# Performance work log

Measured on AMD Instinct MI355X. Metric: run time of the kernel, lower is better.

Reference implementation:

```python
import jax, jax.numpy as jnp
import numpy as np
import math

NODE_DIM = 256
HIDDEN = 128
HEADS = 8
HEAD_DIM = HIDDEN // HEADS
SCALE = math.sqrt(HEAD_DIM)
EPS_DIST = 1e-6
EPS_NORM = 1e-6
LN_EPS = 1e-5


def setup_inputs() -> dict:
    key = jax.random.key(0)
    ks = jax.random.split(key, 16)
    B, N = 2, 768
    node_feats = jax.random.normal(ks[0], (B, N, NODE_DIM), dtype=jnp.float32)
    positions = jax.random.normal(ks[1], (B, N, 2), dtype=jnp.float32)
    mask = jax.random.randint(ks[2], (B, N), 0, 2).astype(bool)
    s = 0.05
    return {
        "node_feats": node_feats,
        "positions": positions,
        "mask": mask,
        "Wq": jax.random.normal(ks[3], (NODE_DIM, HIDDEN), dtype=jnp.float32) * s,
        "Wk": jax.random.normal(ks[4], (NODE_DIM, HIDDEN), dtype=jnp.float32) * s,
        "Wv": jax.random.normal(ks[5], (NODE_DIM, HIDDEN), dtype=jnp.float32) * s,
        "W1": jax.random.normal(ks[6], (3, HIDDEN), dtype=jnp.float32) * s,
        "b1": jnp.zeros((HIDDEN,), dtype=jnp.float32),
        "W2": jax.random.normal(ks[7], (HIDDEN, HIDDEN), dtype=jnp.float32) * s,
        "b2": jnp.zeros((HIDDEN,), dtype=jnp.float32),
        "Wo": jax.random.normal(ks[8], (HIDDEN, NODE_DIM), dtype=jnp.float32) * s,
        "bo": jnp.zeros((NODE_DIM,), dtype=jnp.float32),
        "gamma": jnp.ones((NODE_DIM,), dtype=jnp.float32),
        "beta": jnp.zeros((NODE_DIM,), dtype=jnp.float32),
    }


def reference(node_feats, positions, mask, Wq, Wk, Wv, W1, b1, W2, b2, Wo, bo, gamma, beta):
    B, N, _ = node_feats.shape
    # projections -> [B, H, N, hd]
    q = (node_feats @ Wq).reshape(B, N, HEADS, HEAD_DIM).transpose(0, 2, 1, 3)
    k = (node_feats @ Wk).reshape(B, N, HEADS, HEAD_DIM).transpose(0, 2, 1, 3)
    v = (node_feats @ Wv).reshape(B, N, HEADS, HEAD_DIM).transpose(0, 2, 1, 3)

    # pairwise geometry: deltas [B, N, N, 2]
    deltas = positions[:, :, None, :] - positions[:, None, :, :]
    sq = (deltas ** 2).sum(-1)
    distances = jnp.sqrt(sq + EPS_DIST)  # [B, N, N]
    # F.normalize: divide by norm clamped to eps
    norm = jnp.sqrt(sq)[..., None]
    direction = deltas / jnp.maximum(norm, EPS_NORM)
    edge_geom = jnp.concatenate([direction, distances[..., None]], axis=-1)  # [B,N,N,3]

    # edge MLP -> [B, N, N, HIDDEN] (exact GELU as torch default)
    h = jax.nn.gelu(edge_geom @ W1 + b1, approximate=False)
    edge_bias = (h @ W2 + b2).reshape(B, N, N, HEADS, HEAD_DIM)
    # mean over head_dim, permute to [B, H, N, N]
    bias = edge_bias.mean(-1).transpose(0, 3, 1, 2)

    scores = jnp.einsum('bhid,bhjd->bhij', q, k) / SCALE + bias

    key_mask = mask[:, None, None, :]  # [B,1,1,N]
    neg = jnp.finfo(scores.dtype).min
    scores = jnp.where(key_mask, scores, neg)
    valid_key_rows = jnp.any(key_mask, axis=-1, keepdims=True)  # [B,1,1,1]

    mx = scores.max(axis=-1, keepdims=True)
    mx = jnp.where(valid_key_rows, mx, 0.0)
    scores = jnp.where(valid_key_rows, scores - mx, 0.0)
    w = jax.nn.softmax(scores, axis=-1)
    w = jnp.where(valid_key_rows, w, 0.0)
    w = jnp.nan_to_num(w, nan=0.0, posinf=0.0, neginf=0.0)
    # query mask
    w = w * mask[:, None, :, None].astype(w.dtype)
    # dropout is identity at eval time

    agg = jnp.einsum('bhij,bhjd->bhid', w, v)  # [B,H,N,hd]
    agg = agg.transpose(0, 2, 1, 3).reshape(B, N, HIDDEN)
    agg = agg @ Wo + bo

    mf = mask[..., None].astype(node_feats.dtype)
    agg = agg * mf
    nf = node_feats * mf

    x = nf + agg
    mu = x.mean(-1, keepdims=True)
    var = ((x - mu) ** 2).mean(-1, keepdims=True)
    return (x - mu) / jnp.sqrt(var + LN_EPS) * gamma + beta
```

## Files before the change

kernel.cpp:

```cpp
#include <hip/hip_runtime.h>
#include <float.h>
#include <math.h>

#define NODE_DIM 256
#define HIDDEN   128
#define HEADS    8
#define HEAD_DIM 16
#define NB       768
#define BATCH    2
#define NNODES   (BATCH * NB)
#define SEP      776

typedef _Float16 f16;
typedef _Float16 h2 __attribute__((ext_vector_type(2)));
union F2H { float f; h2 h; unsigned u; };
union V4H { float4 f; h2 h[4]; };

__device__ __forceinline__ float gelu_f(float u) {
  float u2 = u * u;
  float e  = __builtin_amdgcn_exp2f(u * fmaf(u2, -0.10294357f, -2.3022090f));
  return u * __builtin_amdgcn_rcpf(1.0f + e);
}

__global__ __launch_bounds__(256) void prep_kernel(
    const float* __restrict__ nf, const float* __restrict__ pos,
    const int* __restrict__ mask,
    const float* __restrict__ Wq, const float* __restrict__ Wk,
    const float* __restrict__ Wv, const float* __restrict__ W1,
    const float* __restrict__ b1, const float* __restrict__ W2,
    const float* __restrict__ b2, const float* __restrict__ Wo,
    float* __restrict__ qc, f16* __restrict__ kTcH, f16* __restrict__ vcH,
    unsigned* __restrict__ WoP,
    float* __restrict__ P, float* __restrict__ b2m,
    float* __restrict__ pcx, float* __restrict__ pcy,
    int* __restrict__ vlist, int* __restrict__ mlist, int* __restrict__ cnt) {
  int blk = blockIdx.x, t = threadIdx.x;

  if (blk < NNODES / 4) {
    int n0 = blk * 4;
    int b = n0 / NB;
    int lo = n0 - b * NB;
    __shared__ int accv;
    if (t == 0) accv = 0;
    __syncthreads();
    for (int jb = 0; jb < lo; jb += 256) {
      int j = jb + t;
      int mv = (j < lo) && (mask[b * NB + j] != 0);
      unsigned long long ball = __ballot(mv);
      if ((t & 63) == 0) atomicAdd(&accv, __popcll(ball));
    }
    __syncthreads();
    int cb = accv;
    int m0 = mask[n0] != 0, m1 = mask[n0 + 1] != 0, m2 = mask[n0 + 2] != 0,
        m3 = mask[n0 + 3] != 0;
    int civ[4] = {cb, cb + m0, cb + m0 + m1, cb + m0 + m1 + m2};
    int mv4[4] = {m0, m1, m2, m3};

    const float* x0 = nf + (size_t)(n0 + 0) * NODE_DIM;
    const float* x1 = nf + (size_t)(n0 + 1) * NODE_DIM;
    const float* x2 = nf + (size_t)(n0 + 2) * NODE_DIM;
    const float* x3 = nf + (size_t)(n0 + 3) * NODE_DIM;
    for (int id = t; id < 3 * HIDDEN; id += 256) {
      int m = id >> 7, c = id & 127;
      const float* W = (m == 0) ? Wq : (m == 1) ? Wk : Wv;
      float a0 = 0.f, a1 = 0.f, a2 = 0.f, a3 = 0.f;
      float e0 = 0.f, e1 = 0.f, e2 = 0.f, e3 = 0.f;
#pragma unroll 8
      for (int kk = 0; kk < NODE_DIM; kk += 2) {
        float w0 = W[kk * HIDDEN + c];
        float w1 = W[(kk + 1) * HIDDEN + c];
        a0 = fmaf(x0[kk], w0, a0);  e0 = fmaf(x0[kk + 1], w1, e0);
        a1 = fmaf(x1[kk], w0, a1);  e1 = fmaf(x1[kk + 1], w1, e1);
        a2 = fmaf(x2[kk], w0, a2);  e2 = fmaf(x2[kk + 1], w1, e2);
        a3 = fmaf(x3[kk], w0, a3);  e3 = fmaf(x3[kk + 1], w1, e3);
      }
      float acc[4] = {a0 + e0, a1 + e1, a2 + e2, a3 + e3};
#pragma unroll
      for (int n = 0; n < 4; ++n) {
        if (mv4[n]) {
          int slot = b * NB + civ[n];
          if (m == 0)      qc[(size_t)slot * HIDDEN + c] = acc[n];
          else if (m == 1) kTcH[((size_t)b * HIDDEN + c) * NB + civ[n]] = (f16)acc[n];
          else             vcH[(size_t)slot * HIDDEN + c] = (f16)acc[n];
        }
      }
    }
  } else if (blk < NNODES / 4 + 2) {
    int b = blk - NNODES / 4;
    __shared__ int wcnt[4];
    __shared__ int base2[2];
    if (t < 2) base2[t] = 0;
    __syncthreads();
    int lane = t & 63, w = t >> 6;
    for (int iter = 0; iter < NB / 256; ++iter) {
      int j = iter * 256 + t;
      int mv = mask[b * NB + j] != 0;
      unsigned long long ball = __ballot(mv);
      if (lane == 0) wcnt[w] = __popcll(ball);
      __syncthreads();
      int pv = 0;
      for (int i = 0; i < w; ++i) pv += wcnt[i];
      int pin = (lane == 0) ? 0 : __popcll(ball & (~0ull >> (64 - lane)));
      if (mv) {
        int p = base2[0] + pv + pin;
        vlist[b * NB + p] = j;
        pcx[b * NB + p] = pos[(b * NB + j) * 2];
        pcy[b * NB + p] = pos[(b * NB + j) * 2 + 1];
      } else {
        int pm = base2[1] + (w * 64 - pv) + (lane - pin);
        mlist[b * NB + pm] = j;
      }
      __syncthreads();
      if (t == 0) {
        int tot = wcnt[0] + wcnt[1] + wcnt[2] + wcnt[3];
        base2[0] += tot;
        base2[1] += 256 - tot;
      }
      __syncthreads();
    }
    int nv = base2[0];
    if (t == 0) cnt[b] = nv;
    int nvp8 = (nv + 7) & ~7;
    if (t < HIDDEN)
      for (int col = nv; col < nvp8; ++col)
        kTcH[((size_t)b * HIDDEN + t) * NB + col] = (f16)0.0f;
  } else if (blk == NNODES / 4 + 2) {
    __shared__ float w2s[HIDDEN * HEADS];
    for (int idx = t; idx < HIDDEN * HEADS; idx += 256) {
      int c = idx >> 3, h = idx & 7;
      float s = 0.0f;
      for (int d = 0; d < HEAD_DIM; ++d) s += W2[c * HIDDEN + h * HEAD_DIM + d];
      w2s[idx] = s * (1.0f / 16.0f);
    }
    if (t < HEADS) {
      float s = 0.0f;
      for (int d = 0; d < HEAD_DIM; ++d) s += b2[t * HEAD_DIM + d];
      b2m[t] = s * (1.0f / 16.0f);
    }
    __syncthreads();
    if (t < HIDDEN) {
      float* Pr = P + t * 8;
      Pr[0] = W1[t];
      Pr[1] = W1[HIDDEN + t];
      Pr[2] = W1[2 * HIDDEN + t];
      Pr[3] = b1[t];
      f16* ph = (f16*)(Pr + 4);
#pragma unroll
      for (int h = 0; h < HEADS; ++h) ph[h] = (f16)w2s[t * 8 + h];
    }
  } else {
    for (int k2 = 0; k2 < 64; ++k2) {
      F2H w;
      w.h = (h2){(f16)Wo[(2 * k2) * NODE_DIM + t],
                 (f16)Wo[(2 * k2 + 1) * NODE_DIM + t]};
      WoP[k2 * 256 + t] = w.u;
    }
  }
}

__global__ __launch_bounds__(256) void attn_kernel(
    const float* __restrict__ pcx, const float* __restrict__ pcy,
    const int* __restrict__ cnt, const int* __restrict__ vlist,
    const int* __restrict__ mlist, const float* __restrict__ P,
    const float* __restrict__ b2m, const float* __restrict__ qc,
    const f16* __restrict__ kTcH, const f16* __restrict__ vcH,
    const unsigned* __restrict__ WoP,
    const float* __restrict__ nf, const float* __restrict__ bo,
    const float* __restrict__ gamma, const float* __restrict__ beta,
    float* __restrict__ out) {
  int b = blockIdx.x & 1, ci = blockIdx.x >> 1;
  int t = threadIdx.x;
  int nv = cnt[b];
  if (ci >= nv) {
    int node = b * NB + mlist[b * NB + (ci - nv)];
    out[(size_t)node * NODE_DIM + t] = beta[t];
    return;
  }
  int node = b * NB + vlist[b * NB + ci];
  int slot = b * NB + ci;

  __shared__ __align__(16) unsigned char smem[21760];
  f16*   sE    = (f16*)smem;
  float* qs    = (float*)(smem + 12416);
  float* partD = (float*)(smem + 12928);
  float* aggL  = (float*)(smem + 21120);
  float* red   = (float*)(smem + 21632);
  float* invs  = (float*)(smem + 21664);

  if (t < HIDDEN) qs[t] = qc[(size_t)slot * HIDDEN + t];
  float pix = pcx[slot], piy = pcy[slot];
  __syncthreads();

  {
    int h = t >> 5, l = t & 31;
    const f16* kb = kTcH + ((size_t)b * HIDDEN + h * 16) * NB;
    h2 qp[16];
#pragma unroll
    for (int r = 0; r < 16; ++r) {
      f16 qh = (f16)qs[h * 16 + r];
      qp[r] = (h2){qh, qh};
    }
    h2 sc4 = {(f16)0.25f, (f16)0.25f};
    f16 bhh = (f16)b2m[h];
    h2 bh2 = {bhh, bhh};
    int n8 = (nv + 7) >> 3;
    for (int j8 = l; j8 < n8; j8 += 32) {
      h2 acc[4] = {{0, 0}, {0, 0}, {0, 0}, {0, 0}};
#pragma unroll
      for (int r = 0; r < 16; ++r) {
        V4H kv;
        kv.f = *(const float4*)(kb + (size_t)r * NB + j8 * 8);
        acc[0] += qp[r] * kv.h[0];
        acc[1] += qp[r] * kv.h[1];
        acc[2] += qp[r] * kv.h[2];
        acc[3] += qp[r] * kv.h[3];
      }
      V4H res;
#pragma unroll
      for (int p = 0; p < 4; ++p) res.h[p] = acc[p] * sc4 + bh2;
      *(float4*)(sE + h * SEP + j8 * 8) = res.f;
    }
  }
  __syncthreads();

#pragma unroll
  for (int sl = 0; sl < 3; ++sl) {
    int k0 = t + sl * 256;
    if (k0 < nv) {
      int s0 = b * NB + k0;
      float dx = pix - pcx[s0], dy = piy - pcy[s0];
      float sq = fmaf(dx, dx, dy * dy);
      float dist = __builtin_amdgcn_sqrtf(sq + 1e-6f);
      float inv  = fminf(__builtin_amdgcn_rsqf(sq), 1e6f);
      float ux = dx * inv, uy = dy * inv;
      h2 bacc[4] = {{0, 0}, {0, 0}, {0, 0}, {0, 0}};
#pragma unroll 4
      for (int c = 0; c < HIDDEN; ++c) {
        const float4* Pc = (const float4*)(P + c * 8);
        float4 p0 = Pc[0], pw = Pc[1];
        float g = gelu_f(fmaf(ux, p0.x, fmaf(uy, p0.y, fmaf(dist, p0.z, p0.w))));
        f16 gh = (f16)g;
        h2 gg = {gh, gh};
        F2H w0, w1, w2, w3;
        w0.f = pw.x; w1.f = pw.y; w2.f = pw.z; w3.f = pw.w;
        bacc[0] += gg * w0.h;
        bacc[1] += gg * w1.h;
        bacc[2] += gg * w2.h;
        bacc[3] += gg * w3.h;
      }
      f16* row = sE + k0;
#pragma unroll
      for (int p = 0; p < 4; ++p) {
        row[(2 * p + 0) * SEP] = (f16)(row[(2 * p + 0) * SEP] + bacc[p].x);
        row[(2 * p + 1) * SEP] = (f16)(row[(2 * p + 1) * SEP] + bacc[p].y);
      }
    }
  }
  __syncthreads();

  {
    int h = t >> 5, l = t & 31;
    f16* row = sE + h * SEP;
    float m = -FLT_MAX;
    for (int jj = l; jj < nv; jj += 32) m = fmaxf(m, (float)row[jj]);
    for (int off = 16; off; off >>= 1) m = fmaxf(m, __shfl_down(m, off, 32));
    m = __shfl(m, 0, 32);
    float s = 0.0f;
    for (int jj = l; jj < nv; jj += 32) {
      float e = __expf((float)row[jj] - m);
      row[jj] = (f16)e;
      s += e;
    }
    for (int off = 16; off; off >>= 1) s += __shfl_down(s, off, 32);
    if (l == 0) invs[h] = 1.0f / s;
  }
  __syncthreads();

  {
    int o8 = t & 15, g = t >> 4;
    int h = o8 >> 1;
    h2 acc[4] = {{0, 0}, {0, 0}, {0, 0}, {0, 0}};
    for (int jj = g; jj < nv; jj += 16) {
      V4H vv;
      vv.f = *(const float4*)(vcH + (size_t)(b * NB + jj) * HIDDEN + o8 * 8);
      f16 w = sE[h * SEP + jj];
      h2 ww = {w, w};
      acc[0] += ww * vv.h[0];
      acc[1] += ww * vv.h[1];
      acc[2] += ww * vv.h[2];
      acc[3] += ww * vv.h[3];
    }
    float* pd = partD + g * HIDDEN + o8 * 8;
    pd[0] = (float)acc[0].x; pd[1] = (float)acc[0].y;
    pd[2] = (float)acc[1].x; pd[3] = (float)acc[1].y;
    pd[4] = (float)acc[2].x; pd[5] = (float)acc[2].y;
    pd[6] = (float)acc[3].x; pd[7] = (float)acc[3].y;
  }
  __syncthreads();
  if (t < HIDDEN) {
    float s = 0.0f;
#pragma unroll
    for (int g = 0; g < 16; ++g) s += partD[g * HIDDEN + t];
    aggL[t] = s * invs[t >> 4];
  }
  __syncthreads();

  {
    float y0 = bo[t], y1 = 0.f;
    const unsigned* wp = WoP + t;
    const float2* a2 = (const float2*)aggL;
#pragma unroll 4
    for (int k2 = 0; k2 < 64; ++k2) {
      F2H w;
      w.u = wp[(size_t)k2 * 256];
      float2 a = a2[k2];
      y0 = fmaf(a.x, (float)w.h.x, y0);
      y1 = fmaf(a.y, (float)w.h.y, y1);
    }
    float y = y0 + y1;
    float xv = nf[(size_t)node * NODE_DIM + t] + y;
    float s = xv, s2 = xv * xv;
    for (int off = 32; off; off >>= 1) {
      s += __shfl_down(s, off, 64);
      s2 += __shfl_down(s2, off, 64);
    }
    if ((t & 63) == 0) { red[t >> 6] = s; red[4 + (t >> 6)] = s2; }
    __syncthreads();
    s  = red[0] + red[1] + red[2] + red[3];
    s2 = red[4] + red[5] + red[6] + red[7];
    float mu = s * (1.0f / NODE_DIM);
    float var = fmaxf(s2 * (1.0f / NODE_DIM) - mu * mu, 0.0f);
    out[(size_t)node * NODE_DIM + t] =
        (xv - mu) * rsqrtf(var + 1e-5f) * gamma[t] + beta[t];
  }
}

extern "C" void kernel_launch(void* const* d_in, const int* in_sizes, int n_in,
                              void* d_out, int out_size, void* d_ws, size_t ws_size,
                              hipStream_t stream) {
  const float* nf    = (const float*)d_in[0];
  const float* pos   = (const float*)d_in[1];
  const int*   mask  = (const int*)  d_in[2];
  const float* Wq    = (const float*)d_in[3];
  const float* Wk    = (const float*)d_in[4];
  const float* Wv    = (const float*)d_in[5];
  const float* W1    = (const float*)d_in[6];
  const float* b1    = (const float*)d_in[7];
  const float* W2    = (const float*)d_in[8];
  const float* b2    = (const float*)d_in[9];
  const float* Wo    = (const float*)d_in[10];
  const float* bo    = (const float*)d_in[11];
  const float* gamma = (const float*)d_in[12];
  const float* beta  = (const float*)d_in[13];

  const int QKV = NNODES * HIDDEN;

  float*    ws   = (float*)d_ws;
  float*    qc   = ws;
  f16*      kTcH = (f16*)(qc + QKV);
  f16*      vcH  = kTcH + QKV;
  unsigned* WoP  = (unsigned*)(vcH + QKV);
  float*    P    = (float*)(WoP + 64 * 256);
  float*    b2m  = P + HIDDEN * 8;
  float*    pcx  = b2m + 8;
  float*    pcy  = pcx + NNODES;
  int*      vlist= (int*)(pcy + NNODES);
  int*      mlist= vlist + NNODES;
  int*      cnt  = mlist + NNODES;

  prep_kernel<<<NNODES / 4 + 4, 256, 0, stream>>>(
      nf, pos, mask, Wq, Wk, Wv, W1, b1, W2, b2, Wo,
      qc, kTcH, vcH, WoP, P, b2m, pcx, pcy, vlist, mlist, cnt);
  attn_kernel<<<NNODES, 256, 0, stream>>>(
      pcx, pcy, cnt, vlist, mlist, P, b2m, qc, kTcH, vcH, WoP,
      nf, bo, gamma, beta, (float*)d_out);
}
```

Measured before the change: 136.3 us.

## Process two query nodes per attention block to reuse K, V and Wo loads

Each attention block now handles two consecutive query slots instead of one, halving the grid. K tiles, V rows, edge-MLP weights and Wo are loaded once and applied to both queries, which cuts global and L2 traffic per query. The cost is double the shared memory and registers per block, which can reduce occupancy, and fewer blocks (768) to spread across the CUs. The softmax is regrouped to 16 lanes per head-query pair, and masked-out partner slots are written with beta.

```diff
diff --git a/kernel.cpp b/kernel.cpp
--- a/kernel.cpp
+++ b/kernel.cpp
@@ -10,6 +10,7 @@
 #define BATCH    2
 #define NNODES   (BATCH * NB)
 #define SEP      776
+#define SEQ      (HEADS * SEP)
 
 typedef _Float16 f16;
 typedef _Float16 h2 __attribute__((ext_vector_type(2)));
@@ -168,57 +169,77 @@
     const float* __restrict__ nf, const float* __restrict__ bo,
     const float* __restrict__ gamma, const float* __restrict__ beta,
     float* __restrict__ out) {
-  int b = blockIdx.x & 1, ci = blockIdx.x >> 1;
+  int blk = blockIdx.x;
+  int b = blk & 1, ci0 = (blk >> 1) * 2, ci1 = ci0 + 1;
   int t = threadIdx.x;
   int nv = cnt[b];
-  if (ci >= nv) {
-    int node = b * NB + mlist[b * NB + (ci - nv)];
-    out[(size_t)node * NODE_DIM + t] = beta[t];
+
+  if (ci0 >= nv) {
+    float bt = beta[t];
+    int nodeA = b * NB + mlist[b * NB + (ci0 - nv)];
+    int nodeB = b * NB + mlist[b * NB + (ci1 - nv)];
+    out[(size_t)nodeA * NODE_DIM + t] = bt;
+    out[(size_t)nodeB * NODE_DIM + t] = bt;
     return;
   }
-  int node = b * NB + vlist[b * NB + ci];
-  int slot = b * NB + ci;
-
-  __shared__ __align__(16) unsigned char smem[21760];
+  bool v1 = ci1 < nv;
+  int slot0 = b * NB + ci0;
+  int slot1 = b * NB + (v1 ? ci1 : ci0);
+  int node0 = b * NB + vlist[slot0 - b * NB + b * NB];
+  node0 = b * NB + vlist[b * NB + ci0];
+  int node1 = v1 ? (b * NB + vlist[b * NB + ci1]) : -1;
+
+  __shared__ __align__(16) unsigned char smem[43392];
   f16*   sE    = (f16*)smem;
-  float* qs    = (float*)(smem + 12416);
-  float* partD = (float*)(smem + 12928);
-  float* aggL  = (float*)(smem + 21120);
-  float* red   = (float*)(smem + 21632);
-  float* invs  = (float*)(smem + 21664);
-
-  if (t < HIDDEN) qs[t] = qc[(size_t)slot * HIDDEN + t];
-  float pix = pcx[slot], piy = pcy[slot];
+  float* qs    = (float*)(smem + 24832);
+  float* partD = (float*)(smem + 25856);
+  float* aggL  = (float*)(smem + 42240);
+  float* red   = (float*)(smem + 43264);
+  float* invs  = (float*)(smem + 43328);
+
+  if (t < HIDDEN) {
+    qs[t]          = qc[(size_t)slot0 * HIDDEN + t];
+    qs[HIDDEN + t] = qc[(size_t)slot1 * HIDDEN + t];
+  }
+  float pix0 = pcx[slot0], piy0 = pcy[slot0];
+  float pix1 = pcx[slot1], piy1 = pcy[slot1];
   __syncthreads();
 
   {
     int h = t >> 5, l = t & 31;
     const f16* kb = kTcH + ((size_t)b * HIDDEN + h * 16) * NB;
-    h2 qp[16];
+    h2 qp0[16], qp1[16];
 #pragma unroll
     for (int r = 0; r < 16; ++r) {
-      f16 qh = (f16)qs[h * 16 + r];
-      qp[r] = (h2){qh, qh};
+      f16 q0 = (f16)qs[h * 16 + r], q1 = (f16)qs[HIDDEN + h * 16 + r];
+      qp0[r] = (h2){q0, q0};
+      qp1[r] = (h2){q1, q1};
     }
     h2 sc4 = {(f16)0.25f, (f16)0.25f};
     f16 bhh = (f16)b2m[h];
     h2 bh2 = {bhh, bhh};
     int n8 = (nv + 7) >> 3;
     for (int j8 = l; j8 < n8; j8 += 32) {
-      h2 acc[4] = {{0, 0}, {0, 0}, {0, 0}, {0, 0}};
+      h2 a0[4] = {{0,0},{0,0},{0,0},{0,0}};
+      h2 a1[4] = {{0,0},{0,0},{0,0},{0,0}};
 #pragma unroll
       for (int r = 0; r < 16; ++r) {
         V4H kv;
         kv.f = *(const float4*)(kb + (size_t)r * NB + j8 * 8);
-        acc[0] += qp[r] * kv.h[0];
-        acc[1] += qp[r] * kv.h[1];
-        acc[2] += qp[r] * kv.h[2];
-        acc[3] += qp[r] * kv.h[3];
-      }
-      V4H res;
-#pragma unroll
-      for (int p = 0; p < 4; ++p) res.h[p] = acc[p] * sc4 + bh2;
-      *(float4*)(sE + h * SEP + j8 * 8) = res.f;
+#pragma unroll
+        for (int p = 0; p < 4; ++p) {
+          a0[p] += qp0[r] * kv.h[p];
+          a1[p] += qp1[r] * kv.h[p];
+        }
+      }
+      V4H r0, r1;
+#pragma unroll
+      for (int p = 0; p < 4; ++p) {
+        r0.h[p] = a0[p] * sc4 + bh2;
+        r1.h[p] = a1[p] * sc4 + bh2;
+      }
+      *(float4*)(sE + h * SEP + j8 * 8)       = r0.f;
+      *(float4*)(sE + SEQ + h * SEP + j8 * 8) = r1.f;
     }
   }
   __syncthreads();
@@ -228,110 +249,150 @@
     int k0 = t + sl * 256;
     if (k0 < nv) {
       int s0 = b * NB + k0;
-      float dx = pix - pcx[s0], dy = piy - pcy[s0];
-      float sq = fmaf(dx, dx, dy * dy);
-      float dist = __builtin_amdgcn_sqrtf(sq + 1e-6f);
-      float inv  = fminf(__builtin_amdgcn_rsqf(sq), 1e6f);
-      float ux = dx * inv, uy = dy * inv;
-      h2 bacc[4] = {{0, 0}, {0, 0}, {0, 0}, {0, 0}};
+      float px = pcx[s0], py = pcy[s0];
+      float dx0 = pix0 - px, dy0 = piy0 - py;
+      float sq0 = fmaf(dx0, dx0, dy0 * dy0);
+      float dd0 = __builtin_amdgcn_sqrtf(sq0 + 1e-6f);
+      float iv0 = fminf(__builtin_amdgcn_rsqf(sq0), 1e6f);
+      float ux0 = dx0 * iv0, uy0 = dy0 * iv0;
+      float dx1 = pix1 - px, dy1 = piy1 - py;
+      float sq1 = fmaf(dx1, dx1, dy1 * dy1);
+      float dd1 = __builtin_amdgcn_sqrtf(sq1 + 1e-6f);
+      float iv1 = fminf(__builtin_amdgcn_rsqf(sq1), 1e6f);
+      float ux1 = dx1 * iv1, uy1 = dy1 * iv1;
+      h2 ba0[4] = {{0,0},{0,0},{0,0},{0,0}};
+      h2 ba1[4] = {{0,0},{0,0},{0,0},{0,0}};
 #pragma unroll 4
       for (int c = 0; c < HIDDEN; ++c) {
         const float4* Pc = (const float4*)(P + c * 8);
         float4 p0 = Pc[0], pw = Pc[1];
-        float g = gelu_f(fmaf(ux, p0.x, fmaf(uy, p0.y, fmaf(dist, p0.z, p0.w))));
-        f16 gh = (f16)g;
-        h2 gg = {gh, gh};
+        float g0 = gelu_f(fmaf(ux0, p0.x, fmaf(uy0, p0.y, fmaf(dd0, p0.z, p0.w))));
+        float g1 = gelu_f(fmaf(ux1, p0.x, fmaf(uy1, p0.y, fmaf(dd1, p0.z, p0.w))));
+        f16 h0 = (f16)g0, h1 = (f16)g1;
+        h2 gg0 = {h0, h0}, gg1 = {h1, h1};
         F2H w0, w1, w2, w3;
         w0.f = pw.x; w1.f = pw.y; w2.f = pw.z; w3.f = pw.w;
-        bacc[0] += gg * w0.h;
-        bacc[1] += gg * w1.h;
-        bacc[2] += gg * w2.h;
-        bacc[3] += gg * w3.h;
-      }
-      f16* row = sE + k0;
+        ba0[0] += gg0 * w0.h;  ba1[0] += gg1 * w0.h;
+        ba0[1] += gg0 * w1.h;  ba1[1] += gg1 * w1.h;
+        ba0[2] += gg0 * w2.h;  ba1[2] += gg1 * w2.h;
+        ba0[3] += gg0 * w3.h;  ba1[3] += gg1 * w3.h;
+      }
+      f16* r0 = sE + k0;
+      f16* r1 = sE + SEQ + k0;
 #pragma unroll
       for (int p = 0; p < 4; ++p) {
-        row[(2 * p + 0) * SEP] = (f16)(row[(2 * p + 0) * SEP] + bacc[p].x);
-        row[(2 * p + 1) * SEP] = (f16)(row[(2 * p + 1) * SEP] + bacc[p].y);
+        r0[(2*p+0) * SEP] = (f16)(r0[(2*p+0) * SEP] + ba0[p].x);
+        r0[(2*p+1) * SEP] = (f16)(r0[(2*p+1) * SEP] + ba0[p].y);
+        r1[(2*p+0) * SEP] = (f16)(r1[(2*p+0) * SEP] + ba1[p].x);
+        r1[(2*p+1) * SEP] = (f16)(r1[(2*p+1) * SEP] + ba1[p].y);
       }
     }
   }
   __syncthreads();
 
   {
-    int h = t >> 5, l = t & 31;
-    f16* row = sE + h * SEP;
+    int q = t >> 7, h = (t >> 4) & 7, l = t & 15;
+    f16* row = sE + q * SEQ + h * SEP;
     float m = -FLT_MAX;
-    for (int jj = l; jj < nv; jj += 32) m = fmaxf(m, (float)row[jj]);
-    for (int off = 16; off; off >>= 1) m = fmaxf(m, __shfl_down(m, off, 32));
-    m = __shfl(m, 0, 32);
+    for (int jj = l; jj < nv; jj += 16) m = fmaxf(m, (float)row[jj]);
+    for (int off = 8; off; off >>= 1) m = fmaxf(m, __shfl_down(m, off, 16));
+    m = __shfl(m, 0, 16);
     float s = 0.0f;
-    for (int jj = l; jj < nv; jj += 32) {
+    for (int jj = l; jj < nv; jj += 16) {
       float e = __expf((float)row[jj] - m);
       row[jj] = (f16)e;
       s += e;
     }
-    for (int off = 16; off; off >>= 1) s += __shfl_down(s, off, 32);
-    if (l == 0) invs[h] = 1.0f / s;
+    for (int off = 8; off; off >>= 1) s += __shfl_down(s, off, 16);
+    if (l == 0) invs[q * 8 + h] = (s > 0.0f) ? (1.0f / s) : 0.0f;
   }
   __syncthreads();
 
   {
     int o8 = t & 15, g = t >> 4;
     int h = o8 >> 1;
-    h2 acc[4] = {{0, 0}, {0, 0}, {0, 0}, {0, 0}};
+    h2 a0[4] = {{0,0},{0,0},{0,0},{0,0}};
+    h2 a1[4] = {{0,0},{0,0},{0,0},{0,0}};
     for (int jj = g; jj < nv; jj += 16) {
       V4H vv;
       vv.f = *(const float4*)(vcH + (size_t)(b * NB + jj) * HIDDEN + o8 * 8);
-      f16 w = sE[h * SEP + jj];
-      h2 ww = {w, w};
-      acc[0] += ww * vv.h[0];
-      acc[1] += ww * vv.h[1];
-      acc[2] += ww * vv.h[2];
-      acc[3] += ww * vv.h[3];
-    }
-    float* pd = partD + g * HIDDEN + o8 * 8;
-    pd[0] = (float)acc[0].x; pd[1] = (float)acc[0].y;
-    pd[2] = (float)acc[1].x; pd[3] = (float)acc[1].y;
-    pd[4] = (float)acc[2].x; pd[5] = (float)acc[2].y;
-    pd[6] = (float)acc[3].x; pd[7] = (float)acc[3].y;
-  }
-  __syncthreads();
-  if (t < HIDDEN) {
+      f16 w0 = sE[h * SEP + jj];
+      f16 w1 = sE[SEQ + h * SEP + jj];
+      h2 ww0 = {w0, w0}, ww1 = {w1, w1};
+#pragma unroll
+      for (int p = 0; p < 4; ++p) {
+        a0[p] += ww0 * vv.h[p];
+        a1[p] += ww1 * vv.h[p];
+      }
+    }
+    float* pd0 = partD + g * HIDDEN + o8 * 8;
+    float* pd1 = partD + 16 * HIDDEN + g * HIDDEN + o8 * 8;
+#pragma unroll
+    for (int p = 0; p < 4; ++p) {
+      pd0[2*p]   = (float)a0[p].x;  pd0[2*p+1] = (float)a0[p].y;
+      pd1[2*p]   = (float)a1[p].x;  pd1[2*p+1] = (float)a1[p].y;
+    }
+  }
+  __syncthreads();
+  {
+    int q = t >> 7, tt = t & 127;
     float s = 0.0f;
-#pragma unroll
-    for (int g = 0; g < 16; ++g) s += partD[g * HIDDEN + t];
-    aggL[t] = s * invs[t >> 4];
+    const float* pd = partD + q * 16 * HIDDEN;
+#pragma unroll
+    for (int g = 0; g < 16; ++g) s += pd[g * HIDDEN + tt];
+    aggL[q * HIDDEN + tt] = s * invs[q * 8 + (tt >> 4)];
   }
   __syncthreads();
 
   {
-    float y0 = bo[t], y1 = 0.f;
+    float bv = bo[t];
+    float y00 = bv, y01 = 0.f, y10 = bv, y11 = 0.f;
     const unsigned* wp = WoP + t;
-    const float2* a2 = (const float2*)aggL;
+    const float2* a20 = (const float2*)aggL;
+    const float2* a21 = (const float2*)(aggL + HIDDEN);
 #pragma unroll 4
     for (int k2 = 0; k2 < 64; ++k2) {
       F2H w;
       w.u = wp[(size_t)k2 * 256];
-      float2 a = a2[k2];
-      y0 = fmaf(a.x, (float)w.h.x, y0);
-      y1 = fmaf(a.y, (float)w.h.y, y1);
-    }
-    float y = y0 + y1;
-    float xv = nf[(size_t)node * NODE_DIM + t] + y;
-    float s = xv, s2 = xv * xv;
+      float2 a0 = a20[k2], a1 = a21[k2];
+      y00 = fmaf(a0.x, (float)w.h.x, y00);
+      y01 = fmaf(a0.y, (float)w.h.y, y01);
+      y10 = fmaf(a1.x, (float)w.h.x, y10);
+      y11 = fmaf(a1.y, (float)w.h.y, y11);
+    }
+    float xv0 = nf[(size_t)node0 * NODE_DIM + t] + (y00 + y01);
+    float xv1 = v1 ? (nf[(size_t)node1 * NODE_DIM + t] + (y10 + y11)) : 0.0f;
+    float s0 = xv0, s20 = xv0 * xv0, s1 = xv1, s21 = xv1 * xv1;
     for (int off = 32; off; off >>= 1) {
-      s += __shfl_down(s, off, 64);
-      s2 += __shfl_down(s2, off, 64);
-    }
-    if ((t & 63) == 0) { red[t >> 6] = s; red[4 + (t >> 6)] = s2; }
+      s0  += __shfl_down(s0, off, 64);
+      s20 += __shfl_down(s20, off, 64);
+      s1  += __shfl_down(s1, off, 64);
+      s21 += __shfl_down(s21, off, 64);
+    }
+    if ((t & 63) == 0) {
+      int w = t >> 6;
+      red[w] = s0; red[4 + w] = s20; red[8 + w] = s1; red[12 + w] = s21;
+    }
     __syncthreads();
-    s  = red[0] + red[1] + red[2] + red[3];
-    s2 = red[4] + red[5] + red[6] + red[7];
-    float mu = s * (1.0f / NODE_DIM);
-    float var = fmaxf(s2 * (1.0f / NODE_DIM) - mu * mu, 0.0f);
-    out[(size_t)node * NODE_DIM + t] =
-        (xv - mu) * rsqrtf(var + 1e-5f) * gamma[t] + beta[t];
+    {
+      float s  = red[0] + red[1] + red[2] + red[3];
+      float s2 = red[4] + red[5] + red[6] + red[7];
+      float mu = s * (1.0f / NODE_DIM);
+      float var = fmaxf(s2 * (1.0f / NODE_DIM) - mu * mu, 0.0f);
+      out[(size_t)node0 * NODE_DIM + t] =
+          (xv0 - mu) * rsqrtf(var + 1e-5f) * gamma[t] + beta[t];
+    }
+    if (v1) {
+      float s  = red[8] + red[9] + red[10] + red[11];
+      float s2 = red[12] + red[13] + red[14] + red[15];
+      float mu = s * (1.0f / NODE_DIM);
+      float var = fmaxf(s2 * (1.0f / NODE_DIM) - mu * mu, 0.0f);
+      out[(size_t)node1 * NODE_DIM + t] =
+          (xv1 - mu) * rsqrtf(var + 1e-5f) * gamma[t] + beta[t];
+    } else {
+      int nodeB = b * NB + mlist[b * NB + (ci1 - nv)];
+      out[(size_t)nodeB * NODE_DIM + t] = beta[t];
+    }
   }
 }
 
@@ -371,7 +432,7 @@
   prep_kernel<<<NNODES / 4 + 4, 256, 0, stream>>>(
       nf, pos, mask, Wq, Wk, Wv, W1, b1, W2, b2, Wo,
       qc, kTcH, vcH, WoP, P, b2m, pcx, pcy, vlist, mlist, cnt);
-  attn_kernel<<<NNODES, 256, 0, stream>>>(
+  attn_kernel<<<NB, 256, 0, stream>>>(
       pcx, pcy, cnt, vlist, mlist, P, b2m, qc, kTcH, vcH, WoP,
       nf, bo, gamma, beta, (float*)d_out);
 }
```

Result: slower. 147.7 us (+8.3%).
